# Optimization experiments

Hardware: AMD Instinct MI355X
Metric: run time of the kernel (lower is better)

The kernel has to match this reference:

```python
import jax, jax.numpy as jnp
import numpy as np
from jax import lax

CL, IL = 128, 64            # context_length, inst_length (globals in original)
PC, CH1, CH2, CH3 = 64, 128, 256, 256
CK1 = CK2 = CK3 = 3
F1, OUT = 400, 1
B = 4096
C3_OUT = CH3 * (CL - 1 - CK1 - CK2 - CK3 + 3)   # 256*121 = 30976
F1_IN = C3_OUT + CL * IL                        # 39168


def _uni(k, shape, fan_in):
    s = 1.0 / np.sqrt(fan_in)
    return jax.random.uniform(k, shape, jnp.float32, -s, s)


def setup_inputs() -> dict:
    key = jax.random.key(0)
    ks = jax.random.split(key, 14)
    x = jax.random.normal(ks[0], (B, CL * IL), jnp.float32)
    Wp = _uni(ks[1], (PC, IL, 2), IL * 2); bp = _uni(ks[2], (PC,), IL * 2)
    W1 = _uni(ks[3], (CH1, PC, CK1), PC * CK1); b1 = _uni(ks[4], (CH1,), PC * CK1)
    W2 = _uni(ks[5], (CH2, CH1, CK2), CH1 * CK2); b2 = _uni(ks[6], (CH2,), CH1 * CK2)
    W3 = _uni(ks[7], (CH3, CH2, CK3), CH2 * CK3); b3 = _uni(ks[8], (CH3,), CH2 * CK3)
    Wf1 = _uni(ks[9], (F1, F1_IN), F1_IN); bf1 = _uni(ks[10], (F1,), F1_IN)
    Wf2 = _uni(ks[11], (OUT, F1), F1); bf2 = _uni(ks[12], (OUT,), F1)
    return dict(x=x, Wp=Wp, bp=bp, W1=W1, b1=b1, W2=W2, b2=b2,
                W3=W3, b3=b3, Wf1=Wf1, bf1=bf1, Wf2=Wf2, bf2=bf2)


def _conv1d(h, w, b):
    # h: [B,C,L], w: [O,C,K], valid conv, stride 1
    return lax.conv_general_dilated(h, w, (1,), 'VALID',
                                    dimension_numbers=('NCH', 'OIH', 'NCH')) + b[None, :, None]


def reference(x, Wp, bp, W1, b1, W2, b2, W3, b3, Wf1, bf1, Wf2, bf2):
    b = x.shape[0]
    xt = x.reshape(b, CL, IL).transpose(0, 2, 1)          # [B, IL, CL]
    # Fused pairwise convp: original loops i=1..CL-1 over k=2 Conv1d on
    # (x[:,:,0], x[:,:,i]); equivalent to one shared term + one batched matmul.
    base = jnp.einsum('pc,bc->bp', Wp[:, :, 0], xt[:, :, 0])        # [B, PC]
    rest = jnp.einsum('pc,bci->bpi', Wp[:, :, 1], xt[:, :, 1:])     # [B, PC, CL-1]
    h = jax.nn.relu(base[:, :, None] + rest + bp[None, :, None])
    h = jax.nn.relu(_conv1d(h, W1, b1))
    h = jax.nn.relu(_conv1d(h, W2, b2))
    h = jax.nn.relu(_conv1d(h, W3, b3))
    h = h.reshape(b, C3_OUT)
    h = jnp.concatenate([h, xt.reshape(b, IL * CL)], axis=1)        # [B, F1_IN]
    h = jax.nn.relu(h @ Wf1.T + bf1)
    return h @ Wf2.T + bf2
```

## Files before the change

kernel.cpp:

```cpp
#include <hip/hip_runtime.h>


typedef __attribute__((ext_vector_type(8))) short bf16x8;
typedef __attribute__((ext_vector_type(4))) float f32x4;
typedef __attribute__((ext_vector_type(8))) unsigned short u16x8;
typedef __attribute__((ext_vector_type(4))) unsigned short u16x4;
typedef __attribute__((ext_vector_type(2))) unsigned int u32x2;
typedef __attribute__((ext_vector_type(4))) unsigned int u32x4;

#define DEVINL __device__ __forceinline__

DEVINL unsigned short f2bf(float f) {
  unsigned u = __builtin_bit_cast(unsigned, f);
  return (unsigned short)((u + 0x7fffu + ((u >> 16) & 1u)) >> 16);
}
DEVINL float bf2f(unsigned short h) {
  return __builtin_bit_cast(float, ((unsigned)h) << 16);
}
DEVINL unsigned cvtpk(float lo, float hi) {
  unsigned r;
  asm("v_cvt_pk_bf16_f32 %0, %1, %2" : "=v"(r) : "v"(lo), "v"(hi));
  return r;
}
DEVINL f32x4 mfma16(bf16x8 a, bf16x8 b, f32x4 c) {
  return __builtin_amdgcn_mfma_f32_16x16x32_bf16(a, b, c, 0, 0, 0);
}
DEVINL float relu(float v) { return v > 0.f ? v : 0.f; }
DEVINL int sxg(int r, int c, int sh) {
  return (r << sh) + (((c >> 3) ^ (r & 7)) << 3) + (c & 7);
}

constexpr int NB = 4096;

__global__ __launch_bounds__(256) void k_prep_w(
    const float* __restrict__ Wp, const float* __restrict__ W1,
    const float* __restrict__ W2, const float* __restrict__ W3,
    unsigned short* __restrict__ wp1r, unsigned short* __restrict__ wp0r,
    unsigned short* __restrict__ w1p, unsigned short* __restrict__ w2p,
    unsigned short* __restrict__ w3p) {
  int idx = blockIdx.x * 256 + threadIdx.x;
  if (idx < 4096) {
    int p = idx >> 6, i = idx & 63;
    wp1r[p * 64 + i] = f2bf(Wp[(p * 64 + i) * 2 + 1]);
    wp0r[i * 64 + p] = f2bf(Wp[(p * 64 + i) * 2 + 0]);
    return;
  }
  idx -= 4096;
  if (idx < 24576) {
    int f = idx >> 9, l = (idx >> 3) & 63, e = idx & 7;
    int mt = f & 7, t = f >> 3, ks = t & 1, k = t >> 1;
    int o = mt * 16 + (l & 15), c = ks * 32 + (l >> 4) * 8 + e;
    w1p[idx] = f2bf(W1[(o * 64 + c) * 3 + k]);
    return;
  }
  idx -= 24576;
  if (idx < 98304) {
    int f = idx >> 9, l = (idx >> 3) & 63, e = idx & 7;
    int mt = f & 15, t = f >> 4, ks = t & 3, k = t >> 2;
    int o = mt * 16 + (l & 15), c = ks * 32 + (l >> 4) * 8 + e;
    w2p[idx] = f2bf(W2[(o * 128 + c) * 3 + k]);
    return;
  }
  idx -= 98304;
  if (idx < 196608) {
    int f = idx >> 9, l = (idx >> 3) & 63, e = idx & 7;
    int mt = f & 15, t = f >> 4, ks = t & 7, k = t >> 3;
    int o = mt * 16 + (l & 15), c = ks * 32 + (l >> 4) * 8 + e;
    w3p[idx] = f2bf(W3[(o * 256 + c) * 3 + k]);
  }
}

__global__ __launch_bounds__(256) void k_prep_wf1(const float* __restrict__ wf1,
                                                  unsigned short* __restrict__ wf1r) {
  extern __shared__ unsigned short tls[];
  const int m = blockIdx.x / 5, q = blockIdx.x % 5, tid = threadIdx.x;
  unsigned short* dst = wf1r + (size_t)m * 39168;
  if (q < 4) {
    const float* src = wf1 + (size_t)m * 39168 + q * 7744;
    for (int idx = tid; idx < 7744; idx += 256) {
      int o = idx / 121, l = idx - o * 121;
      tls[o * 132 + l] = f2bf(src[idx]);
    }
    __syncthreads();
    for (int idx = tid; idx < 7744; idx += 256) {
      int l = idx >> 6, o = idx & 63;
      dst[l * 256 + q * 64 + o] = tls[o * 132 + l];
    }
  } else {
    const float* src = wf1 + (size_t)m * 39168 + 30976;
    for (int idx = tid; idx < 8192; idx += 256) {
      int il = idx >> 7, cl = idx & 127;
      tls[cl * 66 + il] = f2bf(src[idx]);
    }
    __syncthreads();
    for (int idx = tid; idx < 8192; idx += 256) {
      int cl = idx >> 6, il = idx & 63;
      dst[30976 + idx] = tls[cl * 66 + il];
    }
  }
}

template <int CIN, int COUT, int LIN, int LOUT, int SSHI, int SSHO, bool TOGLB>
DEVINL void conv16(const unsigned short* in_lds,
                   const unsigned short* __restrict__ wpack,
                   const float* __restrict__ bias, unsigned short* out_lds,
                   unsigned short* h3, int b, int lane, int wv) {
  constexpr int KS = CIN / 32;
  constexpr int MT = COUT / 16;
  constexpr int MPW = MT / 4;
  const int lr = lane & 15, lq = lane >> 4;
  const int wm = wv >> 1, wn = wv & 1;
  f32x4 acc[MPW][4];
#pragma unroll
  for (int mi = 0; mi < MPW; ++mi)
#pragma unroll
    for (int ni = 0; ni < 4; ++ni) acc[mi][ni] = (f32x4){0.f, 0.f, 0.f, 0.f};
#pragma unroll
  for (int k = 0; k < 3; ++k)
#pragma unroll
    for (int ks = 0; ks < KS; ++ks) {
      bf16x8 a[MPW];
#pragma unroll
      for (int mi = 0; mi < MPW; ++mi)
        a[mi] = *(const bf16x8*)(wpack +
                                 (((k * KS + ks) * MT + wm * MPW + mi) << 9) +
                                 lane * 8);
      const int col = ks * 32 + lq * 8;
#pragma unroll
      for (int ni = 0; ni < 4; ++ni) {
        int l = (wn * 4 + ni) * 16 + lr + k;
        if (l > LIN - 1) l = LIN - 1;
        bf16x8 bb = *(const bf16x8*)(in_lds + sxg(l, col, SSHI));
#pragma unroll
        for (int mi = 0; mi < MPW; ++mi)
          acc[mi][ni] = mfma16(a[mi], bb, acc[mi][ni]);
      }
    }
#pragma unroll
  for (int mi = 0; mi < MPW; ++mi) {
    const int o0 = (wm * MPW + mi) * 16 + lq * 4;
    const f32x4 bi = *(const f32x4*)(bias + o0);
#pragma unroll
    for (int ni = 0; ni < 4; ++ni) {
      const int l = (wn * 4 + ni) * 16 + lr;
      if (l < LOUT) {
        u32x2 pk;
        pk.x = cvtpk(relu(acc[mi][ni][0] + bi[0]), relu(acc[mi][ni][1] + bi[1]));
        pk.y = cvtpk(relu(acc[mi][ni][2] + bi[2]), relu(acc[mi][ni][3] + bi[3]));
        if constexpr (TOGLB)
          *(u32x2*)(h3 + ((size_t)b * LOUT + l) * COUT + o0) = pk;
        else
          *(u32x2*)(out_lds + sxg(l, o0, SSHO)) = pk;
      }
    }
  }
}

__global__ __launch_bounds__(512, 1) void k_front(
    const float* __restrict__ x, const unsigned short* __restrict__ wp0r,
    const float* __restrict__ bp, const unsigned short* __restrict__ wp1r,
    const unsigned short* __restrict__ w1p, const float* __restrict__ b1,
    const unsigned short* __restrict__ w2p, const float* __restrict__ b2,
    const unsigned short* __restrict__ w3p, const float* __restrict__ b3,
    unsigned short* __restrict__ h3) {
  extern __shared__ unsigned short lds[];
  unsigned short* xs = lds;
  unsigned short* h1s = lds;
  unsigned short* h0s = lds + 16000;
  unsigned short* h2s = lds + 16000;
  __shared__ float pbase[8][64];
  __shared__ float basel[64];
  const int b = blockIdx.x, tid = threadIdx.x;
  const int lane = tid & 63, wv = tid >> 6, lq = lane >> 4, lr = lane & 15;
  const float* xb = x + (size_t)b * 8192;

  for (int idx = tid * 4; idx < 8192; idx += 2048) {
    f32x4 v = *(const f32x4*)(xb + idx);
    int c = idx >> 6, i = idx & 63;
    u32x2 pk;
    pk.x = cvtpk(v[0], v[1]);
    pk.y = cvtpk(v[2], v[3]);
    *(u32x2*)(xs + sxg(c, i, 6)) = pk;
  }
  __syncthreads();

  {
    int p = tid & 63, q = tid >> 6;
    float s = 0.f;
#pragma unroll
    for (int t = 0; t < 8; ++t) {
      int i = q * 8 + t;
      s += bf2f(wp0r[i * 64 + p]) * bf2f(xs[i]);
    }
    pbase[q][p] = s;
  }
  __syncthreads();
  if (tid < 64) {
    float s = bp[tid];
#pragma unroll
    for (int q = 0; q < 8; ++q) s += pbase[q][tid];
    basel[tid] = s;
  }
  __syncthreads();

  {
    const int mt = wv & 3, nh = wv >> 2;
    f32x4 acc[4];
#pragma unroll
    for (int t = 0; t < 4; ++t) acc[t] = (f32x4){0.f, 0.f, 0.f, 0.f};
#pragma unroll
    for (int s = 0; s < 2; ++s) {
      bf16x8 a = *(const bf16x8*)(wp1r + (mt * 16 + lr) * 64 + s * 32 + lq * 8);
#pragma unroll
      for (int t = 0; t < 4; ++t) {
        int j = (nh * 4 + t) * 16 + lr;
        int row = j + 1 > 127 ? 127 : j + 1;
        bf16x8 bb = *(const bf16x8*)(xs + sxg(row, s * 32 + lq * 8, 6));
        acc[t] = mfma16(a, bb, acc[t]);
      }
    }
    const int m0 = mt * 16 + lq * 4;
    f32x4 bl;
#pragma unroll
    for (int r = 0; r < 4; ++r) bl[r] = basel[m0 + r];
#pragma unroll
    for (int t = 0; t < 4; ++t) {
      int j = (nh * 4 + t) * 16 + lr;
      if (j < 127) {
        u32x2 pk;
        pk.x = cvtpk(relu(acc[t][0] + bl[0]), relu(acc[t][1] + bl[1]));
        pk.y = cvtpk(relu(acc[t][2] + bl[2]), relu(acc[t][3] + bl[3]));
        *(u32x2*)(h0s + sxg(j, m0, 6)) = pk;
      }
    }
  }
  __syncthreads();

  conv16<64, 128, 127, 125, 6, 7, false>(h0s, w1p, b1, h1s, nullptr, b, lane, wv);
  __syncthreads();
  conv16<128, 256, 125, 123, 7, 8, false>(h1s, w2p, b2, h2s, nullptr, b, lane, wv);
  __syncthreads();
  conv16<256, 256, 123, 121, 8, 0, true>(h2s, w3p, b3, nullptr, h3, b, lane, wv);
}

__global__ __launch_bounds__(512, 1) void k_fc1(
    const unsigned short* __restrict__ h3, const float* __restrict__ x,
    const unsigned short* __restrict__ wf1r, float* __restrict__ fpart,
    int chunkN, int S) {
  __shared__ unsigned short lB[2][128 * 64];
  const int tid = threadIdx.x;
  const int lane = tid & 63, wv = tid >> 6, lq = lane >> 4, lr = lane & 15;
  const int slice = blockIdx.x % S;
  const int bbase = (blockIdx.x / S) * 128;
  const int per = 612 / S, rem = 612 % S;
  const int c0 = slice * per + (slice < rem ? slice : rem);
  const int c1 = c0 + per + (slice < rem ? 1 : 0);

  f32x4 acc[3][8], acc24;
#pragma unroll
  for (int mi = 0; mi < 3; ++mi)
#pragma unroll
    for (int nt = 0; nt < 8; ++nt) acc[mi][nt] = (f32x4){0.f, 0.f, 0.f, 0.f};
  acc24 = (f32x4){0.f, 0.f, 0.f, 0.f};

  const size_t arow0 = (size_t)((3 * wv + 0) * 16 + lr) * 39168;
  const size_t arow1 = (size_t)((3 * wv + 1) * 16 + lr) * 39168;
  const size_t arow2 = (size_t)((3 * wv + 2) * 16 + lr) * 39168;
  const size_t arow24 = (size_t)(384 + lr) * 39168;

  const int sn0 = tid >> 3, sch0 = tid & 7;
  const int sn1 = (tid + 512) >> 3, sch1 = tid & 7;
  const unsigned short* hrow0 = h3 + (size_t)(bbase + sn0) * 30976 + sch0 * 8;
  const unsigned short* hrow1 = h3 + (size_t)(bbase + sn1) * 30976 + sch1 * 8;
  const float* xrow0 = x + (size_t)(bbase + sn0) * 8192 + sch0 * 8;
  const float* xrow1 = x + (size_t)(bbase + sn1) * 8192 + sch1 * 8;
  const int woff0 = (sn0 << 6) + ((sch0 ^ (sn0 & 7)) << 3);
  const int woff1 = (sn1 << 6) + ((sch1 ^ (sn1 & 7)) << 3);

  u16x8 hv0, hv1;
  f32x4 xv00, xv01, xv10, xv11;
  bool isx;

#define FC1_GLOAD(KC)                                                     \
  {                                                                       \
    const int k0_ = (KC)*64;                                              \
    isx = (k0_ >= 30976);                                                 \
    if (!isx) {                                                           \
      hv0 = *(const u16x8*)(hrow0 + k0_);                                 \
      hv1 = *(const u16x8*)(hrow1 + k0_);                                 \
    } else {                                                              \
      xv00 = *(const f32x4*)(xrow0 + (k0_ - 30976));                      \
      xv01 = *(const f32x4*)(xrow0 + (k0_ - 30976) + 4);                  \
      xv10 = *(const f32x4*)(xrow1 + (k0_ - 30976));                      \
      xv11 = *(const f32x4*)(xrow1 + (k0_ - 30976) + 4);                  \
    }                                                                     \
  }
#define FC1_DSWRITE(BUF)                                                  \
  {                                                                       \
    if (isx) {                                                            \
      _Pragma("unroll") for (int r = 0; r < 4; ++r) {                     \
        hv0[r] = f2bf(xv00[r]);                                           \
        hv0[4 + r] = f2bf(xv01[r]);                                       \
        hv1[r] = f2bf(xv10[r]);                                           \
        hv1[4 + r] = f2bf(xv11[r]);                                       \
      }                                                                   \
    }                                                                     \
    *(u16x8*)(lB[BUF] + woff0) = hv0;                                     \
    *(u16x8*)(lB[BUF] + woff1) = hv1;                                     \
  }
#define FC1_ALOAD(DST, KC)                                                \
  {                                                                       \
    const int ka_ = (KC)*64;                                              \
    _Pragma("unroll") for (int win = 0; win < 2; ++win) {                 \
      const int koff = ka_ + win * 32 + lq * 8;                           \
      DST[win][0] = *(const bf16x8*)(wf1r + arow0 + koff);                \
      DST[win][1] = *(const bf16x8*)(wf1r + arow1 + koff);                \
      DST[win][2] = *(const bf16x8*)(wf1r + arow2 + koff);                \
      DST[win][3] = *(const bf16x8*)(wf1r + arow24 + koff);               \
    }                                                                     \
  }

  bf16x8 aC[2][4], aN[2][4];
  FC1_GLOAD(c0)
  FC1_DSWRITE(0)
  FC1_ALOAD(aC, c0)
  __syncthreads();

#pragma unroll 2
  for (int kc = c0; kc < c1; ++kc) {
    const int p = (kc - c0) & 1;
    const bool more = (kc + 1 < c1);
    if (more) {
      FC1_GLOAD(kc + 1)
      FC1_ALOAD(aN, kc + 1)
    }
#pragma unroll
    for (int win = 0; win < 2; ++win) {
      const int cloc = win * 32 + lq * 8;
#pragma unroll
      for (int nt = 0; nt < 8; ++nt) {
        const int n = nt * 16 + lr;
        bf16x8 bb = *(const bf16x8*)(lB[p] + sxg(n, cloc, 6));
        acc[0][nt] = mfma16(aC[win][0], bb, acc[0][nt]);
        acc[1][nt] = mfma16(aC[win][1], bb, acc[1][nt]);
        acc[2][nt] = mfma16(aC[win][2], bb, acc[2][nt]);
      }
      {
        const int n = wv * 16 + lr;
        bf16x8 bb = *(const bf16x8*)(lB[p] + sxg(n, cloc, 6));
        acc24 = mfma16(aC[win][3], bb, acc24);
      }
    }
    if (more) FC1_DSWRITE(p ^ 1)
    __syncthreads();
#pragma unroll
    for (int w2 = 0; w2 < 2; ++w2)
#pragma unroll
      for (int i = 0; i < 4; ++i) aC[w2][i] = aN[w2][i];
  }
#undef FC1_GLOAD
#undef FC1_DSWRITE
#undef FC1_ALOAD

#pragma unroll
  for (int mi = 0; mi < 3; ++mi) {
    const int m0 = (3 * wv + mi) * 16 + lq * 4;
#pragma unroll
    for (int nt = 0; nt < 8; ++nt) {
      const int bb = bbase + nt * 16 + lr;
      *(f32x4*)(fpart + ((size_t)slice * chunkN + bb) * 400 + m0) = acc[mi][nt];
    }
  }
  {
    const int bb = bbase + wv * 16 + lr;
    *(f32x4*)(fpart + ((size_t)slice * chunkN + bb) * 400 + 384 + lq * 4) = acc24;
  }
}

__global__ __launch_bounds__(256) void k_fc1red(const float* __restrict__ fpart,
                                                const float* __restrict__ bf1,
                                                float* __restrict__ fc,
                                                int chunkN, int S) {
  int idx = blockIdx.x * 256 + threadIdx.x;
  if (idx >= chunkN * 400) return;
  int m = idx % 400;
  float s = bf1[m];
  size_t stride = (size_t)chunkN * 400;
#pragma unroll 4
  for (int sl = 0; sl < S; ++sl) s += fpart[(size_t)sl * stride + idx];
  fc[idx] = relu(s);
}

__global__ __launch_bounds__(256) void k_fc2(const float* __restrict__ fc,
                                             const float* __restrict__ wf2,
                                             const float* __restrict__ bf2,
                                             float* __restrict__ out) {
  int b = blockIdx.x * 4 + (threadIdx.x >> 6);
  int lane = threadIdx.x & 63;
  float s = 0.f;
  for (int m = lane; m < 400; m += 64) s += fc[(size_t)b * 400 + m] * wf2[m];
#pragma unroll
  for (int off = 32; off > 0; off >>= 1) s += __shfl_down(s, off, 64);
  if (lane == 0) out[b] = s + bf2[0];
}

extern "C" void kernel_launch(void* const* d_in, const int* in_sizes, int n_in,
                              void* d_out, int out_size, void* d_ws, size_t ws_size,
                              hipStream_t stream) {
  const float* x = (const float*)d_in[0];
  const float* Wp = (const float*)d_in[1];
  const float* bp = (const float*)d_in[2];
  const float* W1 = (const float*)d_in[3];
  const float* b1 = (const float*)d_in[4];
  const float* W2 = (const float*)d_in[5];
  const float* b2 = (const float*)d_in[6];
  const float* W3 = (const float*)d_in[7];
  const float* b3 = (const float*)d_in[8];
  const float* Wf1 = (const float*)d_in[9];
  const float* bf1 = (const float*)d_in[10];
  const float* Wf2 = (const float*)d_in[11];
  const float* bf2 = (const float*)d_in[12];
  float* out = (float*)d_out;

  const size_t fixed =
      8192 + 8192 + 49152 + 196608 + 393216 + 400ULL * 39168 * 2;
  const int S = 16;
  static const int cand[3] = {2048, 1024, 512};
  int chunkN = 512;
  for (int i = 0; i < 3; ++i) {
    size_t cn = cand[i];
    size_t need = fixed + cn * 61952ULL + (size_t)S * cn * 1600ULL + cn * 1600ULL;
    if (need <= ws_size) {
      chunkN = cand[i];
      break;
    }
  }
  const int nchunk = NB / chunkN;

  char* ws = (char*)d_ws;
  size_t off = 0;
  unsigned short* h3c = (unsigned short*)(ws + off);
  off += (size_t)chunkN * 61952ULL;
  float* fpart = (float*)(ws + off);
  off += (size_t)S * chunkN * 1600ULL;
  float* fc = (float*)(ws + off);
  off += (size_t)chunkN * 1600ULL;
  unsigned short* wp1r = (unsigned short*)(ws + off);
  off += 8192;
  unsigned short* wp0r = (unsigned short*)(ws + off);
  off += 8192;
  unsigned short* w1p = (unsigned short*)(ws + off);
  off += 49152;
  unsigned short* w2p = (unsigned short*)(ws + off);
  off += 196608;
  unsigned short* w3p = (unsigned short*)(ws + off);
  off += 393216;
  unsigned short* wf1r = (unsigned short*)(ws + off);

  k_prep_w<<<1264, 256, 0, stream>>>(Wp, W1, W2, W3, wp1r, wp0r, w1p, w2p, w3p);
  k_prep_wf1<<<2000, 256, 16896, stream>>>(Wf1, wf1r);

  for (int c = 0; c < nchunk; ++c) {
    const float* xc = x + (size_t)c * chunkN * 8192;
    k_front<<<chunkN, 512, 94976, stream>>>(xc, wp0r, bp, wp1r, w1p, b1, w2p,
                                            b2, w3p, b3, h3c);
    k_fc1<<<(chunkN / 128) * S, 512, 0, stream>>>(h3c, xc, wf1r, fpart, chunkN, S);
    k_fc1red<<<(chunkN * 400 + 255) / 256, 256, 0, stream>>>(fpart, bf1, fc,
                                                             chunkN, S);
    k_fc2<<<chunkN / 4, 256, 0, stream>>>(fc, Wf2, bf2, out + (size_t)c * chunkN);
  }
}
```

Measured before the change: 677.6 us.

## Fuse FC1 split-K reduction with FC2 and allow full-batch chunking

Merges the split-K partial-sum reduction with bias and ReLU into the final FC2 dot product, so each wave reduces the 16 slices for one sample and writes one output. This drops the intermediate fc buffer and one kernel launch per chunk. Freeing that buffer also lets the chunk size grow to 4096 when workspace allows, which removes per-chunk launch overhead but needs a larger fpart buffer. Loads in the fused reduction are strided per lane rather than fully coalesced.

```diff
diff --git a/kernel.cpp b/kernel.cpp
--- a/kernel.cpp
+++ b/kernel.cpp
@@ -6,7 +6,6 @@
 typedef __attribute__((ext_vector_type(8))) unsigned short u16x8;
 typedef __attribute__((ext_vector_type(4))) unsigned short u16x4;
 typedef __attribute__((ext_vector_type(2))) unsigned int u32x2;
-typedef __attribute__((ext_vector_type(4))) unsigned int u32x4;
 
 #define DEVINL __device__ __forceinline__
 
@@ -377,31 +376,26 @@
   }
 }
 
-__global__ __launch_bounds__(256) void k_fc1red(const float* __restrict__ fpart,
-                                                const float* __restrict__ bf1,
-                                                float* __restrict__ fc,
-                                                int chunkN, int S) {
-  int idx = blockIdx.x * 256 + threadIdx.x;
-  if (idx >= chunkN * 400) return;
-  int m = idx % 400;
-  float s = bf1[m];
-  size_t stride = (size_t)chunkN * 400;
+__global__ __launch_bounds__(256) void k_tail(const float* __restrict__ fpart,
+                                              const float* __restrict__ bf1,
+                                              const float* __restrict__ wf2,
+                                              const float* __restrict__ bf2,
+                                              float* __restrict__ out,
+                                              int chunkN, int S) {
+  const int b = blockIdx.x * 4 + (threadIdx.x >> 6);
+  const int lane = threadIdx.x & 63;
+  const size_t stride = (size_t)chunkN * 400;
+  float acc = 0.f;
+  for (int m = lane; m < 400; m += 64) {
+    float s = bf1[m];
+    const float* p = fpart + (size_t)b * 400 + m;
 #pragma unroll 4
-  for (int sl = 0; sl < S; ++sl) s += fpart[(size_t)sl * stride + idx];
-  fc[idx] = relu(s);
-}
-
-__global__ __launch_bounds__(256) void k_fc2(const float* __restrict__ fc,
-                                             const float* __restrict__ wf2,
-                                             const float* __restrict__ bf2,
-                                             float* __restrict__ out) {
-  int b = blockIdx.x * 4 + (threadIdx.x >> 6);
-  int lane = threadIdx.x & 63;
-  float s = 0.f;
-  for (int m = lane; m < 400; m += 64) s += fc[(size_t)b * 400 + m] * wf2[m];
-#pragma unroll
-  for (int off = 32; off > 0; off >>= 1) s += __shfl_down(s, off, 64);
-  if (lane == 0) out[b] = s + bf2[0];
+    for (int sl = 0; sl < S; ++sl) s += p[(size_t)sl * stride];
+    acc += relu(s) * wf2[m];
+  }
+#pragma unroll
+  for (int off = 32; off > 0; off >>= 1) acc += __shfl_down(acc, off, 64);
+  if (lane == 0) out[b] = acc + bf2[0];
 }
 
 extern "C" void kernel_launch(void* const* d_in, const int* in_sizes, int n_in,
@@ -425,11 +419,11 @@
   const size_t fixed =
       8192 + 8192 + 49152 + 196608 + 393216 + 400ULL * 39168 * 2;
   const int S = 16;
-  static const int cand[3] = {2048, 1024, 512};
+  static const int cand[4] = {4096, 2048, 1024, 512};
   int chunkN = 512;
-  for (int i = 0; i < 3; ++i) {
+  for (int i = 0; i < 4; ++i) {
     size_t cn = cand[i];
-    size_t need = fixed + cn * 61952ULL + (size_t)S * cn * 1600ULL + cn * 1600ULL;
+    size_t need = fixed + cn * 61952ULL + (size_t)S * cn * 1600ULL;
     if (need <= ws_size) {
       chunkN = cand[i];
       break;
@@ -443,8 +437,6 @@
   off += (size_t)chunkN * 61952ULL;
   float* fpart = (float*)(ws + off);
   off += (size_t)S * chunkN * 1600ULL;
-  float* fc = (float*)(ws + off);
-  off += (size_t)chunkN * 1600ULL;
   unsigned short* wp1r = (unsigned short*)(ws + off);
   off += 8192;
   unsigned short* wp0r = (unsigned short*)(ws + off);
@@ -465,8 +457,7 @@
     k_front<<<chunkN, 512, 94976, stream>>>(xc, wp0r, bp, wp1r, w1p, b1, w2p,
                                             b2, w3p, b3, h3c);
     k_fc1<<<(chunkN / 128) * S, 512, 0, stream>>>(h3c, xc, wf1r, fpart, chunkN, S);
-    k_fc1red<<<(chunkN * 400 + 255) / 256, 256, 0, stream>>>(fpart, bf1, fc,
-                                                             chunkN, S);
-    k_fc2<<<chunkN / 4, 256, 0, stream>>>(fc, Wf2, bf2, out + (size_t)c * chunkN);
-  }
-}
+    k_tail<<<chunkN / 4, 256, 0, stream>>>(fpart, bf1, Wf2, bf2,
+                                           out + (size_t)c * chunkN, chunkN, S);
+  }
+}
```

After: 665.3 us. No clear change (-1.8%).
